# Optimization experiments

Hardware: AMD Instinct MI355X
Metric: run time of the kernel (lower is better)

Reference implementation:

```python
import jax, jax.numpy as jnp
import numpy as np
import math

B, N, H, D = 2, 2048, 16, 64
NUM_BUCKETS, MAX_DIST = 32, 128
MODEL = H * D


def _rel_pos_bucket(rel, num_buckets, max_distance):
    # T5-style bucketing (bidirectional): half the buckets for sign, half log-spaced.
    nb = num_buckets // 2
    ret = (rel >= 0).astype(jnp.int32) * nb
    n = jnp.abs(rel)
    max_exact = nb // 2
    is_small = n < max_exact
    n_safe = jnp.maximum(n, 1).astype(jnp.float32)
    val_large = max_exact + (
        jnp.log(n_safe / max_exact) / math.log(max_distance / max_exact) * (nb - max_exact)
    ).astype(jnp.int32)
    val_large = jnp.minimum(val_large, nb - 1)
    return ret + jnp.where(is_small, n, val_large)


def _rel_pos_bias(rel_emb, n, m):
    q_pos = jnp.arange(m - n, m)
    k_pos = jnp.arange(m)
    rel = k_pos[None, :] - q_pos[:, None]            # [n, m]
    buckets = _rel_pos_bucket(rel, NUM_BUCKETS, MAX_DIST)
    bias = rel_emb[buckets]                          # [n, m, h]
    return bias.transpose(2, 0, 1)[None]             # [1, h, n, m]


def setup_inputs() -> dict:
    key = jax.random.key(0)
    ks = jax.random.split(key, 6)
    return {
        "q": jax.random.normal(ks[0], (B, N, MODEL), dtype=jnp.float32),
        "k": jax.random.normal(ks[1], (B, N, MODEL), dtype=jnp.float32),
        "v": jax.random.normal(ks[2], (B, N, MODEL), dtype=jnp.float32),
        "rel_emb": jax.random.normal(ks[3], (NUM_BUCKETS, H), dtype=jnp.float32) * 0.05,
        "w_out": jax.random.normal(ks[4], (MODEL, MODEL), dtype=jnp.float32) * (MODEL ** -0.5),
        "b_out": jax.random.normal(ks[5], (MODEL,), dtype=jnp.float32) * 0.02,
    }


def reference(q, k, v, rel_emb, w_out, b_out):
    b, n, _ = q.shape
    split = lambda x: x.reshape(b, n, H, D).transpose(0, 2, 1, 3)  # b h n d
    qh, kh, vh = split(q), split(k), split(v)
    sim = jnp.einsum('bhnd,bhmd->bhnm', qh, kh)
    sim = (sim + _rel_pos_bias(rel_emb, n, n)) * (D ** -0.5)  # note: scale AFTER bias, as in source
    attn = jax.nn.softmax(sim, axis=-1)
    out = jnp.einsum('bhnm,bhmd->bhnd', attn, vh)
    out = out.transpose(0, 2, 1, 3).reshape(b, n, H * D)
    return out @ w_out.T + b_out
```

## Files before the change

kernel.cpp:

```cpp
#include <hip/hip_runtime.h>

#define BB 2
#define NN 2048
#define HH 16
#define MODEL 1024
#define CSC 0.18033688011112042f

typedef short bf16x8 __attribute__((ext_vector_type(8)));
typedef float f32x4 __attribute__((ext_vector_type(4)));
typedef int i32x2 __attribute__((ext_vector_type(2)));

__device__ __forceinline__ unsigned short f2bf(float x) {
  unsigned int u = __builtin_bit_cast(unsigned int, x);
  u += 0x7fffu + ((u >> 16) & 1u);
  return (unsigned short)(u >> 16);
}

__device__ __forceinline__ unsigned int pack_bf2(float a, float b) {
  unsigned int ua = __builtin_bit_cast(unsigned int, a) + 0x8000u;
  unsigned int ub = __builtin_bit_cast(unsigned int, b) + 0x8000u;
  return __builtin_amdgcn_perm(ub, ua, 0x07060302u);
}

__device__ __forceinline__ unsigned int pack2_rne(float a, float b) {
  return (unsigned int)f2bf(a) | ((unsigned int)f2bf(b) << 16);
}

__device__ __forceinline__ float fast_exp2(float x) {
#if __has_builtin(__builtin_amdgcn_exp2f)
  return __builtin_amdgcn_exp2f(x);
#else
  return exp2f(x);
#endif
}

__device__ __forceinline__ f32x4 mfma16(bf16x8 a, bf16x8 b, f32x4 c) {
  return __builtin_amdgcn_mfma_f32_16x16x32_bf16(a, b, c, 0, 0, 0);
}

__device__ __forceinline__ void async_copy16(void* lds_base, const void* g) {
  __builtin_amdgcn_global_load_lds(
      (const __attribute__((address_space(1))) void*)g,
      (__attribute__((address_space(3))) void*)lds_base, 16, 0, 0);
}

__global__ void prep_kernel(const float* __restrict__ k, const float* __restrict__ w,
                            const float* __restrict__ v, const float* __restrict__ rel_emb,
                            unsigned short* __restrict__ kb, unsigned short* __restrict__ wb,
                            unsigned short* __restrict__ vt, float* __restrict__ biasTab) {
  __shared__ unsigned short tile[64][65];
  const int blk = blockIdx.x;
  if (blk < 1024) {
    const int kt = blk & 31, bh = blk >> 5;
    const int b = bh >> 4, h = bh & 15;
    const int row = threadIdx.x >> 2, dc = (threadIdx.x & 3) * 16;
    const float* src = k + ((long)(b * NN + kt * 64 + row)) * MODEL + h * 64 + dc;
    float4 f0 = reinterpret_cast<const float4*>(src)[0];
    float4 f1 = reinterpret_cast<const float4*>(src)[1];
    float4 f2 = reinterpret_cast<const float4*>(src)[2];
    float4 f3 = reinterpret_cast<const float4*>(src)[3];
    unsigned short* dst = kb + ((long)blk * 64 + row) * 64 + dc;
    uint4 u0{pack2_rne(f0.x, f0.y), pack2_rne(f0.z, f0.w),
             pack2_rne(f1.x, f1.y), pack2_rne(f1.z, f1.w)};
    uint4 u1{pack2_rne(f2.x, f2.y), pack2_rne(f2.z, f2.w),
             pack2_rne(f3.x, f3.y), pack2_rne(f3.z, f3.w)};
    reinterpret_cast<uint4*>(dst)[0] = u0;
    reinterpret_cast<uint4*>(dst)[1] = u1;
  } else if (blk < 2048) {
    int i = (blk - 1024) * 256 + threadIdx.x;
    float4 f = reinterpret_cast<const float4*>(w)[i];
    ushort4 u;
    u.x = f2bf(f.x); u.y = f2bf(f.y); u.z = f2bf(f.z); u.w = f2bf(f.w);
    reinterpret_cast<ushort4*>(wb)[i] = u;
  } else if (blk < 3072) {
    const int blk2 = blk - 2048;
    const int ntl = blk2 & 31;
    const int n0 = ntl * 64;
    const int bh = blk2 >> 5;
    const int b = bh >> 4, h = bh & 15;
    const int c = threadIdx.x & 63;
    const int r = threadIdx.x >> 6;
#pragma unroll
    for (int i = 0; i < 16; ++i) {
      int nl = r * 16 + i;
      tile[c][nl] = f2bf(v[((long)(b * NN + n0 + nl)) * MODEL + h * 64 + c]);
    }
    __syncthreads();
#pragma unroll
    for (int i = 0; i < 16; ++i) {
      int d = r * 16 + i;
      vt[((long)(bh * 32 + ntl) * 64 + d) * 64 + c] = tile[d][c];
    }
  } else {
    int idx = (blk - 3072) * 256 + threadIdx.x;
    if (idx >= 4095) return;
    int rel = idx - 2047;
    int nn = rel < 0 ? -rel : rel;
    int bucket;
    if (nn < 8) {
      bucket = nn;
    } else {
      float val = logf((float)nn * 0.125f) / logf(16.0f) * 8.0f;
      int vl = 8 + (int)val;
      if (vl > 15) vl = 15;
      bucket = vl;
    }
    if (rel >= 0) bucket += 16;
#pragma unroll
    for (int h = 0; h < 16; ++h)
      biasTab[h * 4095 + idx] = rel_emb[bucket * 16 + h] * CSC - 12.0f;
  }
}

__global__ __launch_bounds__(256, 2) void flash16(
    const float* __restrict__ qf32, const unsigned short* __restrict__ kb,
    const unsigned short* __restrict__ vtb, const float* __restrict__ biasTab,
    unsigned short* __restrict__ attn) {
  __shared__ __align__(16) float obuf[4 * 64 * 68];
  __shared__ __align__(16) float scratch[512];

  const int i = blockIdx.x;
  const int bh = (i & 7) * 4 + ((i >> 3) >> 5);
  const int qt = (i >> 3) & 31;
  const int b = bh >> 4, h = bh & 15;
  const int q0 = qt * 64;
  const int tid = threadIdx.x, w = tid >> 6, lane = tid & 63;
  const int g = lane >> 4, c = lane & 15;

  const float* btab = biasTab + h * 4095 + 2047;
  for (int j = tid; j < 441; j += 256) scratch[j] = btab[j - 220];
  const float cPos = btab[200], cNeg = btab[-200];
  __syncthreads();

  bf16x8 qf0[4], qf1[4];
  const float* qbase = qf32 + ((long)(b * NN + q0)) * MODEL + h * 64;
#pragma unroll
  for (int nt = 0; nt < 4; ++nt) {
    const float* r = qbase + (16 * nt + c) * MODEL + 8 * g;
    float4 f0 = *reinterpret_cast<const float4*>(r);
    float4 f1 = *reinterpret_cast<const float4*>(r + 4);
    float4 f2 = *reinterpret_cast<const float4*>(r + 32);
    float4 f3 = *reinterpret_cast<const float4*>(r + 36);
    qf0[nt] = __builtin_bit_cast(bf16x8, uint4{pack2_rne(f0.x, f0.y), pack2_rne(f0.z, f0.w),
                                               pack2_rne(f1.x, f1.y), pack2_rne(f1.z, f1.w)});
    qf1[nt] = __builtin_bit_cast(bf16x8, uint4{pack2_rne(f2.x, f2.y), pack2_rne(f2.z, f2.w),
                                               pack2_rne(f3.x, f3.y), pack2_rne(f3.z, f3.w)});
  }

  const unsigned short* kbase = kb + (long)bh * 131072;
  const unsigned short* vbase = vtb + (long)bh * 131072;

  f32x4 o[4][4];
  float l_p[4] = {0.f, 0.f, 0.f, 0.f};
#pragma unroll
  for (int mt = 0; mt < 4; ++mt)
#pragma unroll
    for (int nt = 0; nt < 4; ++nt) o[mt][nt] = f32x4{0.f, 0.f, 0.f, 0.f};

  for (int it = 0; it < 8; ++it) {
    const int kt = w + 4 * it;
    bf16x8 kf0[4], kf1[4];
    const unsigned short* krow = kbase + kt * 4096;
#pragma unroll
    for (int mt = 0; mt < 4; ++mt) {
      const unsigned short* r = krow + (16 * mt + c) * 64 + 8 * g;
      kf0[mt] = *reinterpret_cast<const bf16x8*>(r);
      kf1[mt] = *reinterpret_cast<const bf16x8*>(r + 32);
    }
    bf16x8 vf0[4], vf1[4];
    const unsigned short* vrow = vbase + kt * 4096;
#pragma unroll
    for (int mt = 0; mt < 4; ++mt) {
      const unsigned short* r = vrow + (16 * mt + c) * 64 + 8 * g;
      vf0[mt] = *reinterpret_cast<const bf16x8*>(r);
      vf1[mt] = *reinterpret_cast<const bf16x8*>(r + 32);
    }
    const int lo = kt * 64 - q0 - 63, hi = kt * 64 + 63 - q0;
    const bool sat = (lo >= 91 || hi <= -91);
    const float cb = (lo >= 91) ? cPos : cNeg;

#pragma unroll
    for (int nt = 0; nt < 4; ++nt) {
      f32x4 s[4];
      __builtin_amdgcn_s_setprio(1);
#pragma unroll
      for (int mt = 0; mt < 4; ++mt) {
        s[mt] = mfma16(kf0[mt], qf0[nt], f32x4{0.f, 0.f, 0.f, 0.f});
        s[mt] = mfma16(kf1[mt], qf1[nt], s[mt]);
      }
      __builtin_amdgcn_s_setprio(0);
      if (sat) {
#pragma unroll
        for (int mt = 0; mt < 4; ++mt)
#pragma unroll
          for (int rr = 0; rr < 4; ++rr) s[mt][rr] = s[mt][rr] * CSC + cb;
      } else {
        const int base = kt * 64 + 4 * g - q0 - 16 * nt - c + 220;
#pragma unroll
        for (int mt = 0; mt < 4; ++mt)
#pragma unroll
          for (int rr = 0; rr < 4; ++rr)
            s[mt][rr] = s[mt][rr] * CSC + scratch[base + 16 * mt + rr];
      }
      float sum = 0.f;
      unsigned int pk[4][2];
#pragma unroll
      for (int mt = 0; mt < 4; ++mt) {
        const float p0 = fast_exp2(s[mt][0]);
        const float p1 = fast_exp2(s[mt][1]);
        const float p2 = fast_exp2(s[mt][2]);
        const float p3 = fast_exp2(s[mt][3]);
        sum += (p0 + p1) + (p2 + p3);
        pk[mt][0] = pack_bf2(p0, p1);
        pk[mt][1] = pack_bf2(p2, p3);
      }
      l_p[nt] += sum;
      unsigned int d0, d1, d2, d3, d4, d5, d6, d7;
      {
        i32x2 x, y;
        x = __builtin_amdgcn_permlane32_swap((int)pk[0][0], (int)pk[1][0], false, false);
        y = __builtin_amdgcn_permlane16_swap(x[0], x[1], false, false);
        d0 = (unsigned int)y[0]; d2 = (unsigned int)y[1];
        x = __builtin_amdgcn_permlane32_swap((int)pk[0][1], (int)pk[1][1], false, false);
        y = __builtin_amdgcn_permlane16_swap(x[0], x[1], false, false);
        d1 = (unsigned int)y[0]; d3 = (unsigned int)y[1];
        x = __builtin_amdgcn_permlane32_swap((int)pk[2][0], (int)pk[3][0], false, false);
        y = __builtin_amdgcn_permlane16_swap(x[0], x[1], false, false);
        d4 = (unsigned int)y[0]; d6 = (unsigned int)y[1];
        x = __builtin_amdgcn_permlane32_swap((int)pk[2][1], (int)pk[3][1], false, false);
        y = __builtin_amdgcn_permlane16_swap(x[0], x[1], false, false);
        d5 = (unsigned int)y[0]; d7 = (unsigned int)y[1];
      }
      const bf16x8 pb0 = __builtin_bit_cast(bf16x8, uint4{d0, d1, d2, d3});
      const bf16x8 pb1 = __builtin_bit_cast(bf16x8, uint4{d4, d5, d6, d7});
      __builtin_amdgcn_s_setprio(1);
#pragma unroll
      for (int mt = 0; mt < 4; ++mt) {
        o[mt][nt] = mfma16(vf0[mt], pb0, o[mt][nt]);
        o[mt][nt] = mfma16(vf1[mt], pb1, o[mt][nt]);
      }
      __builtin_amdgcn_s_setprio(0);
    }
  }

  __syncthreads();
  float* ob = obuf + w * 64 * 68;
#pragma unroll
  for (int nt = 0; nt < 4; ++nt) {
    ob[(16 * nt + c) * 68 + 64 + g] = l_p[nt];
#pragma unroll
    for (int mt = 0; mt < 4; ++mt)
      *reinterpret_cast<f32x4*>(&ob[(16 * nt + c) * 68 + 16 * mt + 4 * g]) = o[mt][nt];
  }
  __syncthreads();

  const int qr = 16 * w + c;
  float l = 0.f;
#pragma unroll
  for (int u = 0; u < 4; ++u)
#pragma unroll
    for (int gg = 0; gg < 4; ++gg) l += obuf[(u * 64 + qr) * 68 + 64 + gg];
  const float inv = 1.f / l;

  float acc[16];
#pragma unroll
  for (int j = 0; j < 16; ++j) acc[j] = 0.f;
#pragma unroll
  for (int u = 0; u < 4; ++u) {
    const float* src = obuf + (u * 64 + qr) * 68;
    f32x4 r0 = *reinterpret_cast<const f32x4*>(&src[8 * g]);
    f32x4 r1 = *reinterpret_cast<const f32x4*>(&src[8 * g + 4]);
    f32x4 r2 = *reinterpret_cast<const f32x4*>(&src[32 + 8 * g]);
    f32x4 r3 = *reinterpret_cast<const f32x4*>(&src[32 + 8 * g + 4]);
#pragma unroll
    for (int j = 0; j < 4; ++j) {
      acc[j] += r0[j];
      acc[4 + j] += r1[j];
      acc[8 + j] += r2[j];
      acc[12 + j] += r3[j];
    }
  }
  unsigned int od[8];
#pragma unroll
  for (int t = 0; t < 8; ++t) od[t] = pack_bf2(acc[2 * t] * inv, acc[2 * t + 1] * inv);
  unsigned short* orow = attn + ((long)(b * NN + q0 + qr)) * MODEL + h * 64;
  *reinterpret_cast<uint4*>(orow + 8 * g) = uint4{od[0], od[1], od[2], od[3]};
  *reinterpret_cast<uint4*>(orow + 32 + 8 * g) = uint4{od[4], od[5], od[6], od[7]};
}

__global__ void proj_gemm_kernel(const unsigned short* __restrict__ A,
                                 const unsigned short* __restrict__ Bw,
                                 const float* __restrict__ bias,
                                 float* __restrict__ out) {
  __shared__ __align__(16) unsigned short At[2][128 * 64];
  __shared__ __align__(16) unsigned short Bt[2][64 * 64];
  int bm0 = blockIdx.x * 128, bn0 = blockIdx.y * 64;
  int tid = threadIdx.x, w = tid >> 6, lane = tid & 63;
  int g = lane >> 4, c = lane & 15;
  int m0 = (w & 1) * 64, n0 = (w >> 1) * 32;

  f32x4 acc[4][2];
#pragma unroll
  for (int mi = 0; mi < 4; ++mi)
#pragma unroll
    for (int nj = 0; nj < 2; ++nj) acc[mi][nj] = f32x4{0.f, 0.f, 0.f, 0.f};

  int rloc = lane >> 3, p = lane & 7;

  auto stage = [&](int buf, int kt) {
#pragma unroll
    for (int t = 0; t < 4; ++t) {
      int row = w * 32 + t * 8 + rloc;
      async_copy16(&At[buf][(w * 32 + t * 8) * 64],
                   A + (long)(bm0 + row) * 1024 + kt * 64 + (p ^ rloc) * 8);
    }
#pragma unroll
    for (int t = 0; t < 2; ++t) {
      int row = w * 16 + t * 8 + rloc;
      async_copy16(&Bt[buf][(w * 16 + t * 8) * 64],
                   Bw + (long)(bn0 + row) * 1024 + kt * 64 + (p ^ rloc) * 8);
    }
  };

  int cur = 0;
  stage(0, 0);
  for (int kt = 0; kt < 16; ++kt) {
    __syncthreads();
    if (kt < 15) stage(cur ^ 1, kt + 1);

    bf16x8 af0[4], af1[4], bf0[2], bf1[2];
#pragma unroll
    for (int mi = 0; mi < 4; ++mi) {
      int row = m0 + 16 * mi + c, sw = row & 7;
      af0[mi] = *reinterpret_cast<const bf16x8*>(&At[cur][row * 64 + (g ^ sw) * 8]);
      af1[mi] = *reinterpret_cast<const bf16x8*>(&At[cur][row * 64 + ((4 + g) ^ sw) * 8]);
    }
#pragma unroll
    for (int nj = 0; nj < 2; ++nj) {
      int row = n0 + 16 * nj + c, sw = row & 7;
      bf0[nj] = *reinterpret_cast<const bf16x8*>(&Bt[cur][row * 64 + (g ^ sw) * 8]);
      bf1[nj] = *reinterpret_cast<const bf16x8*>(&Bt[cur][row * 64 + ((4 + g) ^ sw) * 8]);
    }
#pragma unroll
    for (int mi = 0; mi < 4; ++mi)
#pragma unroll
      for (int nj = 0; nj < 2; ++nj) {
        acc[mi][nj] = mfma16(af0[mi], bf0[nj], acc[mi][nj]);
        acc[mi][nj] = mfma16(af1[mi], bf1[nj], acc[mi][nj]);
      }
    cur ^= 1;
  }

#pragma unroll
  for (int mi = 0; mi < 4; ++mi)
#pragma unroll
    for (int nj = 0; nj < 2; ++nj)
#pragma unroll
      for (int r = 0; r < 4; ++r) {
        int row = bm0 + m0 + mi * 16 + 4 * g + r;
        int col = bn0 + n0 + nj * 16 + c;
        out[(long)row * 1024 + col] = acc[mi][nj][r] + bias[col];
      }
}

extern "C" void kernel_launch(void* const* d_in, const int* in_sizes, int n_in,
                              void* d_out, int out_size, void* d_ws, size_t ws_size,
                              hipStream_t stream) {
  const float* q = (const float*)d_in[0];
  const float* k = (const float*)d_in[1];
  const float* v = (const float*)d_in[2];
  const float* rel_emb = (const float*)d_in[3];
  const float* w_out = (const float*)d_in[4];
  const float* b_out = (const float*)d_in[5];
  float* out = (float*)d_out;

  char* ws = (char*)d_ws;
  unsigned short* kb   = (unsigned short*)(ws + (8u << 20));
  unsigned short* vt   = (unsigned short*)(ws + (16u << 20));
  unsigned short* attn = (unsigned short*)(ws + (24u << 20));
  unsigned short* wb   = (unsigned short*)(ws + (32u << 20));
  float* biasTab       = (float*)(ws + (34u << 20));

  hipLaunchKernelGGL(prep_kernel, dim3(3089), dim3(256), 0, stream,
                     k, w_out, v, rel_emb, kb, wb, vt, biasTab);
  hipLaunchKernelGGL(flash16, dim3(1024), dim3(256), 0, stream,
                     q, kb, vt, biasTab, attn);
  hipLaunchKernelGGL(proj_gemm_kernel, dim3(32, 16), dim3(256), 0, stream,
                     attn, wb, b_out, out);
}
```

Before: 188.1 us.

## Load projection GEMM operands directly from global memory, dropping LDS staging

The output projection GEMM no longer stages A and W tiles into double-buffered LDS through async global-to-LDS copies. Each wave now loads its bf16 fragments straight from global memory, and the block tile changes to 64 rows by 128 columns, with each wave owning a 64x32 slice. This removes the __syncthreads barriers and the LDS traffic, but gives up cross-wave operand sharing in LDS. The A tile is now read redundantly by all four waves, and W is read with strided per-lane 16-byte loads that depend on L2/L1 caching.

```diff
diff --git a/kernel.cpp b/kernel.cpp
--- a/kernel.cpp
+++ b/kernel.cpp
@@ -36,12 +36,6 @@
 
 __device__ __forceinline__ f32x4 mfma16(bf16x8 a, bf16x8 b, f32x4 c) {
   return __builtin_amdgcn_mfma_f32_16x16x32_bf16(a, b, c, 0, 0, 0);
-}
-
-__device__ __forceinline__ void async_copy16(void* lds_base, const void* g) {
-  __builtin_amdgcn_global_load_lds(
-      (const __attribute__((address_space(1))) void*)g,
-      (__attribute__((address_space(3))) void*)lds_base, 16, 0, 0);
 }
 
 __global__ void prep_kernel(const float* __restrict__ k, const float* __restrict__ w,
@@ -288,16 +282,15 @@
   *reinterpret_cast<uint4*>(orow + 32 + 8 * g) = uint4{od[4], od[5], od[6], od[7]};
 }
 
-__global__ void proj_gemm_kernel(const unsigned short* __restrict__ A,
-                                 const unsigned short* __restrict__ Bw,
-                                 const float* __restrict__ bias,
-                                 float* __restrict__ out) {
-  __shared__ __align__(16) unsigned short At[2][128 * 64];
-  __shared__ __align__(16) unsigned short Bt[2][64 * 64];
-  int bm0 = blockIdx.x * 128, bn0 = blockIdx.y * 64;
-  int tid = threadIdx.x, w = tid >> 6, lane = tid & 63;
-  int g = lane >> 4, c = lane & 15;
-  int m0 = (w & 1) * 64, n0 = (w >> 1) * 32;
+__global__ void proj_gemm_kernel(
+    const unsigned short* __restrict__ A, const unsigned short* __restrict__ Bw,
+    const float* __restrict__ bias, float* __restrict__ out) {
+  const int bx = blockIdx.x;
+  const int by = blockIdx.y;
+  const int tid = threadIdx.x, w = tid >> 6, lane = tid & 63;
+  const int g = lane >> 4, c = lane & 15;
+  const int row0 = bx * 64;
+  const int col0 = by * 128 + w * 32;
 
   f32x4 acc[4][2];
 #pragma unroll
@@ -305,41 +298,23 @@
 #pragma unroll
     for (int nj = 0; nj < 2; ++nj) acc[mi][nj] = f32x4{0.f, 0.f, 0.f, 0.f};
 
-  int rloc = lane >> 3, p = lane & 7;
-
-  auto stage = [&](int buf, int kt) {
-#pragma unroll
-    for (int t = 0; t < 4; ++t) {
-      int row = w * 32 + t * 8 + rloc;
-      async_copy16(&At[buf][(w * 32 + t * 8) * 64],
-                   A + (long)(bm0 + row) * 1024 + kt * 64 + (p ^ rloc) * 8);
-    }
-#pragma unroll
-    for (int t = 0; t < 2; ++t) {
-      int row = w * 16 + t * 8 + rloc;
-      async_copy16(&Bt[buf][(w * 16 + t * 8) * 64],
-                   Bw + (long)(bn0 + row) * 1024 + kt * 64 + (p ^ rloc) * 8);
-    }
-  };
-
-  int cur = 0;
-  stage(0, 0);
+  const unsigned short* arow = A + (long)(row0 + c) * 1024 + 8 * g;
+  const unsigned short* brow = Bw + (long)(col0 + c) * 1024 + 8 * g;
+
   for (int kt = 0; kt < 16; ++kt) {
-    __syncthreads();
-    if (kt < 15) stage(cur ^ 1, kt + 1);
-
+    const int k0 = kt * 64;
     bf16x8 af0[4], af1[4], bf0[2], bf1[2];
 #pragma unroll
     for (int mi = 0; mi < 4; ++mi) {
-      int row = m0 + 16 * mi + c, sw = row & 7;
-      af0[mi] = *reinterpret_cast<const bf16x8*>(&At[cur][row * 64 + (g ^ sw) * 8]);
-      af1[mi] = *reinterpret_cast<const bf16x8*>(&At[cur][row * 64 + ((4 + g) ^ sw) * 8]);
+      const unsigned short* r = arow + (long)(16 * mi) * 1024 + k0;
+      af0[mi] = *reinterpret_cast<const bf16x8*>(r);
+      af1[mi] = *reinterpret_cast<const bf16x8*>(r + 32);
     }
 #pragma unroll
     for (int nj = 0; nj < 2; ++nj) {
-      int row = n0 + 16 * nj + c, sw = row & 7;
-      bf0[nj] = *reinterpret_cast<const bf16x8*>(&Bt[cur][row * 64 + (g ^ sw) * 8]);
-      bf1[nj] = *reinterpret_cast<const bf16x8*>(&Bt[cur][row * 64 + ((4 + g) ^ sw) * 8]);
+      const unsigned short* r = brow + (long)(16 * nj) * 1024 + k0;
+      bf0[nj] = *reinterpret_cast<const bf16x8*>(r);
+      bf1[nj] = *reinterpret_cast<const bf16x8*>(r + 32);
     }
 #pragma unroll
     for (int mi = 0; mi < 4; ++mi)
@@ -348,7 +323,6 @@
         acc[mi][nj] = mfma16(af0[mi], bf0[nj], acc[mi][nj]);
         acc[mi][nj] = mfma16(af1[mi], bf1[nj], acc[mi][nj]);
       }
-    cur ^= 1;
   }
 
 #pragma unroll
@@ -357,8 +331,8 @@
     for (int nj = 0; nj < 2; ++nj)
 #pragma unroll
       for (int r = 0; r < 4; ++r) {
-        int row = bm0 + m0 + mi * 16 + 4 * g + r;
-        int col = bn0 + n0 + nj * 16 + c;
+        int row = row0 + mi * 16 + 4 * g + r;
+        int col = col0 + nj * 16 + c;
         out[(long)row * 1024 + col] = acc[mi][nj][r] + bias[col];
       }
 }
@@ -385,6 +359,6 @@
                      k, w_out, v, rel_emb, kb, wb, vt, biasTab);
   hipLaunchKernelGGL(flash16, dim3(1024), dim3(256), 0, stream,
                      q, kb, vt, biasTab, attn);
-  hipLaunchKernelGGL(proj_gemm_kernel, dim3(32, 16), dim3(256), 0, stream,
+  hipLaunchKernelGGL(proj_gemm_kernel, dim3(64, 8), dim3(256), 0, stream,
                      attn, wb, b_out, out);
 }
```

After: 216.9 us. +15.3%, slower.
